# Kernel tuning notes

Measured on AMD Instinct MI355X. Metric: run time of the kernel, lower is better.

Reference implementation:

```python
import jax, jax.numpy as jnp
import numpy as np

D_MODEL = 2048
NUM_HEADS = 16
HEAD_DIM = D_MODEL // NUM_HEADS


def _rotary(x, head_dim):
    # x: (..., T, head_dim). Matches torch module: half-split rotation.
    T = x.shape[-2]
    pos = jnp.arange(T, dtype=jnp.float32)[:, None]              # (T,1)
    dim = jnp.arange(head_dim // 2, dtype=jnp.float32)[None, :]  # (1,hd/2)
    angle = pos * (1.0 / jnp.power(10000.0, 2.0 * dim / head_dim))
    cos = jnp.cos(angle)  # (T, hd/2), broadcasts over leading dims
    sin = jnp.sin(angle)
    x1 = x[..., : head_dim // 2]
    x2 = x[..., head_dim // 2:]
    return jnp.concatenate([x1 * cos - x2 * sin, x2 * cos + x1 * sin], axis=-1)


def setup_inputs() -> dict:
    key = jax.random.key(0)
    ks = jax.random.split(key, 9)
    B, T, D, H, HD = 2, 2048, D_MODEL, NUM_HEADS, HEAD_DIM
    s = 1.0 / np.sqrt(D)
    return {
        "x": jax.random.normal(ks[0], (B, T, D), jnp.float32),
        "Wq": jax.random.normal(ks[1], (D, D), jnp.float32) * s,
        "bq": jnp.zeros((D,), jnp.float32),
        "Wk": jax.random.normal(ks[2], (D, HD), jnp.float32) * s,
        "bk": jnp.zeros((HD,), jnp.float32),
        "Wv": jax.random.normal(ks[3], (D, HD), jnp.float32) * s,
        "bv": jnp.zeros((HD,), jnp.float32),
        "Wo": jax.random.normal(ks[4], (D, D), jnp.float32) * s,
        "bo": jnp.zeros((D,), jnp.float32),
    }


def reference(x, Wq, bq, Wk, bk, Wv, bv, Wo, bo):
    B, T, D = x.shape
    H, HD = NUM_HEADS, HEAD_DIM
    q = (x @ Wq + bq).reshape(B, T, H, HD).transpose(0, 2, 1, 3)  # (B,H,T,hd)
    k = (x @ Wk + bk)[:, None]                                    # (B,1,T,hd)
    v = (x @ Wv + bv)[:, None]                                    # (B,1,T,hd)
    q = _rotary(q, HD)
    k = _rotary(k, HD)
    scores = jnp.einsum("bhqd,bhkd->bhqk", q, jnp.broadcast_to(k, (B, 1, T, HD))) / jnp.sqrt(jnp.float32(HD))
    attn = jax.nn.softmax(scores, axis=-1)                        # (B,H,T,T)
    ctx = jnp.einsum("bhqk,bhkd->bhqd", attn, jnp.broadcast_to(v, (B, 1, T, HD)))
    ctx = ctx.transpose(0, 2, 1, 3).reshape(B, T, D)
    return ctx @ Wo + bo
```

## Files before the change

### kernel.cpp

```cpp
#include <hip/hip_runtime.h>
#include <math.h>

#define T_SEQ  2048
#define DMODEL 2048
#define NHEADS 16
#define HDIM   128
#define MROWS  4096

typedef __attribute__((ext_vector_type(8)))  __bf16 bf16x8;
typedef __attribute__((ext_vector_type(4)))  __bf16 bf16x4;
typedef __attribute__((ext_vector_type(4)))  float  f32x4;
typedef __attribute__((ext_vector_type(16))) float  f32x16;

#define GLOBAL_AS __attribute__((address_space(1)))
#define LDS_AS    __attribute__((address_space(3)))
__device__ __forceinline__ void async_copy16(const __bf16* g, __bf16* l) {
  __builtin_amdgcn_global_load_lds((const GLOBAL_AS void*)g, (LDS_AS void*)l, 16, 0, 0);
}

__global__ void build_rope_kernel(float2* __restrict__ rope) {
  int idx = blockIdx.x * blockDim.x + threadIdx.x;
  int d = idx & 63, pos = idx >> 6;
  double freq = pow(10000.0, -(double)d / 64.0);
  double ang = (double)pos * freq;
  rope[idx] = make_float2((float)cos(ang), (float)sin(ang));
}

__global__ void cast_bf16_kernel(const float* __restrict__ in,
                                 __bf16* __restrict__ out, int n4) {
  int i = blockIdx.x * blockDim.x + threadIdx.x;
  if (i >= n4) return;
  float4 v = ((const float4*)in)[i];
  bf16x4 o = { (__bf16)v.x, (__bf16)v.y, (__bf16)v.z, (__bf16)v.w };
  *(bf16x4*)(out + (size_t)i*4) = o;
}

__global__ void wtrans_kernel(const float* __restrict__ Wq,
                              const float* __restrict__ Wk,
                              const float* __restrict__ Wv,
                              const float* __restrict__ Wo,
                              __bf16* __restrict__ wqkvt,
                              __bf16* __restrict__ wot) {
  __shared__ float t[32][33];
  const int bx = blockIdx.x;
  const float* src; __bf16* dst; int istride, c0, orow;
  if (bx < 64)       { src = Wq; istride = 2048; c0 = bx*32;      orow = c0;        dst = wqkvt; }
  else if (bx < 68)  { src = Wk; istride = 128;  c0 = (bx-64)*32; orow = 2048 + c0; dst = wqkvt; }
  else if (bx < 72)  { src = Wv; istride = 128;  c0 = (bx-68)*32; orow = 2176 + c0; dst = wqkvt; }
  else               { src = Wo; istride = 2048; c0 = (bx-72)*32; orow = c0;        dst = wot; }
  const int tx = threadIdx.x & 31, ty = threadIdx.x >> 5;
  const int r0 = blockIdx.y*32;
#pragma unroll
  for (int i = 0; i < 4; ++i)
    t[ty + i*8][tx] = src[(size_t)(r0 + ty + i*8)*istride + c0 + tx];
  __syncthreads();
#pragma unroll
  for (int i = 0; i < 4; ++i)
    dst[(size_t)(orow + ty + i*8)*2048 + r0 + tx] = (__bf16)t[tx][ty + i*8];
}

__global__ void transpose_v_kernel(const __bf16* __restrict__ in,
                                   __bf16* __restrict__ out) {
  __shared__ __bf16 t[32][34];
  const int bz = blockIdx.z;
  in  += (size_t)bz * 2048 * 128;
  out += (size_t)bz * 128 * 2048;
  const int tx = threadIdx.x & 31, ty = threadIdx.x >> 5;
  const int r0 = blockIdx.y*32, c0 = blockIdx.x*32;
#pragma unroll
  for (int i = 0; i < 4; ++i)
    t[ty + i*8][tx] = in[(size_t)(r0 + ty + i*8)*128 + c0 + tx];
  __syncthreads();
#pragma unroll
  for (int i = 0; i < 4; ++i)
    out[(size_t)(c0 + ty + i*8)*2048 + r0 + tx] = t[tx][ty + i*8];
}

__global__ __launch_bounds__(256) void gemm_qkv_fused(
    const __bf16* __restrict__ A,
    const __bf16* __restrict__ Bt,
    const float* __restrict__ bq, const float* __restrict__ bk,
    const float* __restrict__ bv,
    const float2* __restrict__ rope,
    __bf16* __restrict__ qrb,
    __bf16* __restrict__ kbb,
    __bf16* __restrict__ vbb,
    float qscale)
{
  __shared__ __bf16 As[128*32];
  __shared__ __bf16 Bs[128*32];
  const int tid = threadIdx.x;
  const int lane = tid & 63, wave = tid >> 6;
  const int quad = lane >> 4, l16 = lane & 15;
  const int m0 = (wave >> 1)*64, n0 = (wave & 1)*32;
  const int row0 = blockIdx.y*128, col0 = blockIdx.x*128;
  const int srow = lane >> 2, scol = (lane & 3)*8;

  f32x4 acc[4][4];
#pragma unroll
  for (int i = 0; i < 4; ++i)
#pragma unroll
    for (int j = 0; j < 4; ++j) acc[i][j] = (f32x4){0.f,0.f,0.f,0.f};

  const __bf16* Ag = A  + (size_t)(row0 + wave*32 + srow)*DMODEL + scol;
  const __bf16* Bg = Bt + (size_t)(col0 + wave*32 + srow)*DMODEL + scol;
  __bf16* AsW = &As[wave*1024];
  __bf16* BsW = &Bs[wave*1024];

  for (int kk = 0; kk < DMODEL; kk += 32) {
    __syncthreads();
    async_copy16(Ag + kk,                     AsW);
    async_copy16(Ag + kk + (size_t)16*DMODEL, AsW + 512);
    async_copy16(Bg + kk,                     BsW);
    async_copy16(Bg + kk + (size_t)16*DMODEL, BsW + 512);
    __syncthreads();
    bf16x8 af[4], bfr[4];
#pragma unroll
    for (int i = 0; i < 4; ++i)
      af[i] = *(const bf16x8*)&As[(m0 + i*16 + l16)*32 + quad*8];
#pragma unroll
    for (int j = 0; j < 4; ++j) {
      const int cb = n0 + (j & 1)*16 + (j >> 1)*64;
      bfr[j] = *(const bf16x8*)&Bs[(cb + l16)*32 + quad*8];
    }
#pragma unroll
    for (int i = 0; i < 4; ++i)
#pragma unroll
      for (int j = 0; j < 4; ++j)
        acc[i][j] = __builtin_amdgcn_mfma_f32_16x16x32_bf16(af[i], bfr[j], acc[i][j], 0,0,0);
  }

  const int bx = blockIdx.x;
  const float* bias_p; float scale; bool rot; __bf16* obase; int ostride;
  if (bx < 16)      { bias_p = bq + bx*128; scale = qscale; rot = true;
                      obase = qrb + bx*128; ostride = 2048; }
  else if (bx == 16){ bias_p = bk; scale = 1.f; rot = true;
                      obase = kbb; ostride = 128; }
  else              { bias_p = bv; scale = 1.f; rot = false;
                      obase = vbb; ostride = 128; }

#pragma unroll
  for (int j = 0; j < 2; ++j) {
    const int d = n0 + j*16 + l16;
    const float b1 = bias_p[d], b2 = bias_p[d + 64];
#pragma unroll
    for (int i = 0; i < 4; ++i) {
      const int rl = m0 + i*16 + quad*4;
#pragma unroll
      for (int r = 0; r < 4; ++r) {
        const int rg = row0 + rl + r;
        const float x1 = acc[i][j][r]   + b1;
        const float x2 = acc[i][j+2][r] + b2;
        float c = 1.f, s = 0.f;
        if (rot) { float2 cs = rope[(size_t)(rg & (T_SEQ-1))*64 + d]; c = cs.x; s = cs.y; }
        obase[(size_t)rg*ostride + d]      = (__bf16)((x1*c - x2*s)*scale);
        obase[(size_t)rg*ostride + d + 64] = (__bf16)((x2*c + x1*s)*scale);
      }
    }
  }
}

__global__ __launch_bounds__(256) void gemm_bf16_t128(
    const __bf16* __restrict__ A, const __bf16* __restrict__ Bt,
    const float* __restrict__ bias, float* __restrict__ C,
    int M, int N, int K)
{
  __shared__ __bf16 As[128*32];
  __shared__ __bf16 Bs[128*32];
  const int tid = threadIdx.x;
  const int lane = tid & 63, wave = tid >> 6;
  const int quad = lane >> 4, l16 = lane & 15;
  const int m0 = (wave & 1)*64, n0 = (wave >> 1)*64;
  const int row0 = blockIdx.y*128, col0 = blockIdx.x*128;
  const int srow = lane >> 2, scol = (lane & 3)*8;

  f32x4 acc[4][4];
#pragma unroll
  for (int i = 0; i < 4; ++i)
#pragma unroll
    for (int j = 0; j < 4; ++j) acc[i][j] = (f32x4){0.f,0.f,0.f,0.f};

  const __bf16* Ag = A  + (size_t)(row0 + wave*32 + srow)*K + scol;
  const __bf16* Bg = Bt + (size_t)(col0 + wave*32 + srow)*K + scol;
  __bf16* AsW = &As[wave*1024];
  __bf16* BsW = &Bs[wave*1024];

  for (int kk = 0; kk < K; kk += 32) {
    __syncthreads();
    async_copy16(Ag + kk,              AsW);
    async_copy16(Ag + kk + (size_t)16*K, AsW + 512);
    async_copy16(Bg + kk,              BsW);
    async_copy16(Bg + kk + (size_t)16*K, BsW + 512);
    __syncthreads();
    bf16x8 af[4], bfr[4];
#pragma unroll
    for (int i = 0; i < 4; ++i)
      af[i] = *(const bf16x8*)&As[(m0 + i*16 + l16)*32 + quad*8];
#pragma unroll
    for (int j = 0; j < 4; ++j)
      bfr[j] = *(const bf16x8*)&Bs[(n0 + j*16 + l16)*32 + quad*8];
#pragma unroll
    for (int i = 0; i < 4; ++i)
#pragma unroll
      for (int j = 0; j < 4; ++j)
        acc[i][j] = __builtin_amdgcn_mfma_f32_16x16x32_bf16(af[i], bfr[j], acc[i][j], 0,0,0);
  }
#pragma unroll
  for (int j = 0; j < 4; ++j) {
    const int ccol = col0 + n0 + j*16 + l16;
    const float bvv = bias[ccol];
#pragma unroll
    for (int i = 0; i < 4; ++i) {
      const int crow = row0 + m0 + i*16 + quad*4;
#pragma unroll
      for (int r = 0; r < 4; ++r)
        C[(size_t)(crow + r)*N + ccol] = acc[i][j][r] + bvv;
    }
  }
}

#define KSTR 136
#define VSTR 72
#define PSTR 72
__global__ __launch_bounds__(256) void mqa_attn_mfma(
    const __bf16* __restrict__ qb,
    const __bf16* __restrict__ kb,
    const __bf16* __restrict__ vt,
    __bf16* __restrict__ ctx)
{
  __shared__ __bf16 Ks[64*KSTR];
  __shared__ __bf16 Vs[128*VSTR];
  __shared__ __bf16 Ps[4][32*PSTR];
  __shared__ float  Linv[128];
  const int tid = threadIdx.x, lane = tid & 63, wave = tid >> 6;
  const int h5 = lane >> 5, l32 = lane & 31;
  const int h = blockIdx.y, b = blockIdx.z;
  const int qbase = blockIdx.x*128 + wave*32;

  bf16x8 qf[8];
  const __bf16* qp = qb + ((size_t)b*T_SEQ + qbase + l32)*DMODEL + h*HDIM;
#pragma unroll
  for (int ds = 0; ds < 8; ++ds) qf[ds] = *(const bf16x8*)(qp + ds*16 + h5*8);

  f32x16 oacc[4];
#pragma unroll
  for (int g = 0; g < 4; ++g)
#pragma unroll
    for (int r = 0; r < 16; ++r) oacc[g][r] = 0.f;
  float lsum = 0.f;

  const __bf16* kbase = kb + (size_t)b*T_SEQ*HDIM;
  const __bf16* vbase = vt + (size_t)b*HDIM*T_SEQ;

  for (int kt = 0; kt < T_SEQ/64; ++kt) {
    __syncthreads();
#pragma unroll
    for (int i = 0; i < 4; ++i) {
      int idx = i*256 + tid;
      int key = idx >> 4, c = idx & 15;
      *(bf16x8*)&Ks[key*KSTR + c*8] =
          *(const bf16x8*)(kbase + (size_t)(kt*64 + key)*HDIM + c*8);
    }
#pragma unroll
    for (int i = 0; i < 4; ++i) {
      int idx = i*256 + tid;
      int d = idx >> 3, c = idx & 7;
      *(bf16x8*)&Vs[d*VSTR + c*8] =
          *(const bf16x8*)(vbase + (size_t)d*T_SEQ + kt*64 + c*8);
    }
    __syncthreads();

    f32x16 sacc[2];
#pragma unroll
    for (int kg = 0; kg < 2; ++kg) {
#pragma unroll
      for (int r = 0; r < 16; ++r) sacc[kg][r] = 0.f;
#pragma unroll
      for (int ds = 0; ds < 8; ++ds) {
        bf16x8 kf = *(const bf16x8*)&Ks[(kg*32 + l32)*KSTR + ds*16 + h5*8];
        sacc[kg] = __builtin_amdgcn_mfma_f32_32x32x16_bf16(kf, qf[ds], sacc[kg], 0,0,0);
      }
    }
#pragma unroll
    for (int kg = 0; kg < 2; ++kg)
#pragma unroll
      for (int r1 = 0; r1 < 4; ++r1) {
        bf16x4 pk;
#pragma unroll
        for (int r0 = 0; r0 < 4; ++r0) {
          float p = __builtin_amdgcn_exp2f(sacc[kg][r1*4 + r0]);
          lsum += p;
          pk[r0] = (__bf16)p;
        }
        *(bf16x4*)&Ps[wave][l32*PSTR + kg*32 + r1*8 + h5*4] = pk;
      }
    __asm__ volatile("s_waitcnt lgkmcnt(0)" ::: "memory");
#pragma unroll
    for (int ks = 0; ks < 4; ++ks) {
      bf16x8 pf = *(const bf16x8*)&Ps[wave][l32*PSTR + ks*16 + h5*8];
#pragma unroll
      for (int g = 0; g < 4; ++g) {
        bf16x8 vf = *(const bf16x8*)&Vs[(g*32 + l32)*VSTR + ks*16 + h5*8];
        oacc[g] = __builtin_amdgcn_mfma_f32_32x32x16_bf16(pf, vf, oacc[g], 0,0,0);
      }
    }
  }

  lsum += __shfl_xor(lsum, 32);
  if (h5 == 0) Linv[wave*32 + l32] = 1.f / lsum;
  __asm__ volatile("s_waitcnt lgkmcnt(0)" ::: "memory");

  __bf16* op = ctx + ((size_t)b*T_SEQ + qbase)*DMODEL + h*HDIM + l32;
#pragma unroll
  for (int r1 = 0; r1 < 4; ++r1) {
    float4 iv = *(const float4*)&Linv[wave*32 + r1*8 + h5*4];
#pragma unroll
    for (int r0 = 0; r0 < 4; ++r0) {
      int qrow = r1*8 + h5*4 + r0;
#pragma unroll
      for (int g = 0; g < 4; ++g)
        op[(size_t)qrow*DMODEL + g*32] = (__bf16)(oacc[g][r1*4 + r0] * (&iv.x)[r0]);
    }
  }
}

extern "C" void kernel_launch(void* const* d_in, const int* in_sizes, int n_in,
                              void* d_out, int out_size, void* d_ws, size_t ws_size,
                              hipStream_t stream) {
  const float* x  = (const float*)d_in[0];
  const float* Wq = (const float*)d_in[1];
  const float* bq = (const float*)d_in[2];
  const float* Wk = (const float*)d_in[3];
  const float* bk = (const float*)d_in[4];
  const float* Wv = (const float*)d_in[5];
  const float* bv = (const float*)d_in[6];
  const float* Wo = (const float*)d_in[7];
  const float* bo = (const float*)d_in[8];
  float* out = (float*)d_out;

  uint8_t* ws = (uint8_t*)d_ws;
  __bf16* qrb  = (__bf16*)(ws);
  __bf16* xb   = (__bf16*)(ws + 16777216);
  __bf16* wqkvt= (__bf16*)(ws + 33554432);
  __bf16* wot  = (__bf16*)(ws + 42991616);
  __bf16* kbb  = (__bf16*)(ws + 51380224);
  __bf16* vbb  = (__bf16*)(ws + 52428800);
  __bf16* vtb  = (__bf16*)(ws + 53477376);
  float2* rope = (float2*)(ws + 54525952);

  const float qscale = 1.4426950408889634f * 0.08838834764831845f;

  build_rope_kernel<<<512, 256, 0, stream>>>(rope);
  wtrans_kernel<<<dim3(136,64), 256, 0, stream>>>(Wq, Wk, Wv, Wo, wqkvt, wot);
  cast_bf16_kernel<<<8192, 256, 0, stream>>>(x, xb, MROWS*DMODEL/4);

  gemm_qkv_fused<<<dim3(18,32), 256, 0, stream>>>(
      xb, wqkvt, bq, bk, bv, rope, qrb, kbb, vbb, qscale);

  transpose_v_kernel<<<dim3(4,64,2), 256, 0, stream>>>(vbb, vtb);

  mqa_attn_mfma<<<dim3(16,16,2), 256, 0, stream>>>(qrb, kbb, vtb, xb);

  gemm_bf16_t128<<<dim3(16,32), 256, 0, stream>>>(xb, wot, bo, out, MROWS, DMODEL, DMODEL);
}
```

Before: 314.0 us.

## Keep attention probabilities in registers via permuted K rows, drop LDS P staging

The K-tile row index is permuted so the S=K·Q^T MFMA output layout lines up with the B-operand layout needed for the P·V MFMA. The exp'd scores then go straight from registers into the PV product, and the transposed product O^T=V^T·P^T is accumulated. This removes the per-tile LDS write/read of P and its waitcnt barrier. The epilogue becomes per-query-row vectorized bf16x4 stores without the Linv LDS exchange. Correctness depends on the bit permutation exactly matching the MFMA register layouts.

```diff
diff --git a/kernel.cpp b/kernel.cpp
--- a/kernel.cpp
+++ b/kernel.cpp
@@ -221,7 +221,6 @@
 
 #define KSTR 136
 #define VSTR 72
-#define PSTR 72
 __global__ __launch_bounds__(256) void mqa_attn_mfma(
     const __bf16* __restrict__ qb,
     const __bf16* __restrict__ kb,
@@ -230,10 +229,9 @@
 {
   __shared__ __bf16 Ks[64*KSTR];
   __shared__ __bf16 Vs[128*VSTR];
-  __shared__ __bf16 Ps[4][32*PSTR];
-  __shared__ float  Linv[128];
   const int tid = threadIdx.x, lane = tid & 63, wave = tid >> 6;
   const int h5 = lane >> 5, l32 = lane & 31;
+  const int swr = (l32 & 19) | ((l32 & 4) << 1) | ((l32 & 8) >> 1);
   const int h = blockIdx.y, b = blockIdx.z;
   const int qbase = blockIdx.x*128 + wave*32;
 
@@ -270,58 +268,46 @@
     }
     __syncthreads();
 
-    f32x16 sacc[2];
 #pragma unroll
     for (int kg = 0; kg < 2; ++kg) {
-#pragma unroll
-      for (int r = 0; r < 16; ++r) sacc[kg][r] = 0.f;
+      f32x16 sacc;
+#pragma unroll
+      for (int r = 0; r < 16; ++r) sacc[r] = 0.f;
 #pragma unroll
       for (int ds = 0; ds < 8; ++ds) {
-        bf16x8 kf = *(const bf16x8*)&Ks[(kg*32 + l32)*KSTR + ds*16 + h5*8];
-        sacc[kg] = __builtin_amdgcn_mfma_f32_32x32x16_bf16(kf, qf[ds], sacc[kg], 0,0,0);
+        bf16x8 kf = *(const bf16x8*)&Ks[(kg*32 + swr)*KSTR + ds*16 + h5*8];
+        sacc = __builtin_amdgcn_mfma_f32_32x32x16_bf16(kf, qf[ds], sacc, 0,0,0);
       }
-    }
-#pragma unroll
-    for (int kg = 0; kg < 2; ++kg)
-#pragma unroll
-      for (int r1 = 0; r1 < 4; ++r1) {
-        bf16x4 pk;
-#pragma unroll
-        for (int r0 = 0; r0 < 4; ++r0) {
-          float p = __builtin_amdgcn_exp2f(sacc[kg][r1*4 + r0]);
-          lsum += p;
-          pk[r0] = (__bf16)p;
+      bf16x8 pf[2];
+#pragma unroll
+      for (int r = 0; r < 16; ++r) {
+        float p = __builtin_amdgcn_exp2f(sacc[r]);
+        lsum += p;
+        pf[r >> 3][r & 7] = (__bf16)p;
+      }
+#pragma unroll
+      for (int ks = 0; ks < 2; ++ks)
+#pragma unroll
+        for (int g = 0; g < 4; ++g) {
+          bf16x8 vf = *(const bf16x8*)&Vs[(g*32 + l32)*VSTR + kg*32 + ks*16 + h5*8];
+          oacc[g] = __builtin_amdgcn_mfma_f32_32x32x16_bf16(vf, pf[ks], oacc[g], 0,0,0);
         }
-        *(bf16x4*)&Ps[wave][l32*PSTR + kg*32 + r1*8 + h5*4] = pk;
-      }
-    __asm__ volatile("s_waitcnt lgkmcnt(0)" ::: "memory");
-#pragma unroll
-    for (int ks = 0; ks < 4; ++ks) {
-      bf16x8 pf = *(const bf16x8*)&Ps[wave][l32*PSTR + ks*16 + h5*8];
-#pragma unroll
-      for (int g = 0; g < 4; ++g) {
-        bf16x8 vf = *(const bf16x8*)&Vs[(g*32 + l32)*VSTR + ks*16 + h5*8];
-        oacc[g] = __builtin_amdgcn_mfma_f32_32x32x16_bf16(pf, vf, oacc[g], 0,0,0);
-      }
     }
   }
 
   lsum += __shfl_xor(lsum, 32);
-  if (h5 == 0) Linv[wave*32 + l32] = 1.f / lsum;
-  __asm__ volatile("s_waitcnt lgkmcnt(0)" ::: "memory");
-
-  __bf16* op = ctx + ((size_t)b*T_SEQ + qbase)*DMODEL + h*HDIM + l32;
-#pragma unroll
-  for (int r1 = 0; r1 < 4; ++r1) {
-    float4 iv = *(const float4*)&Linv[wave*32 + r1*8 + h5*4];
-#pragma unroll
-    for (int r0 = 0; r0 < 4; ++r0) {
-      int qrow = r1*8 + h5*4 + r0;
-#pragma unroll
-      for (int g = 0; g < 4; ++g)
-        op[(size_t)qrow*DMODEL + g*32] = (__bf16)(oacc[g][r1*4 + r0] * (&iv.x)[r0]);
-    }
-  }
+  const float inv = 1.f / lsum;
+
+  __bf16* op = ctx + ((size_t)b*T_SEQ + qbase + l32)*DMODEL + h*HDIM;
+#pragma unroll
+  for (int g = 0; g < 4; ++g)
+#pragma unroll
+    for (int rq = 0; rq < 4; ++rq) {
+      const int d = g*32 + rq*8 + h5*4;
+      bf16x4 ov = { (__bf16)(oacc[g][rq*4+0]*inv), (__bf16)(oacc[g][rq*4+1]*inv),
+                    (__bf16)(oacc[g][rq*4+2]*inv), (__bf16)(oacc[g][rq*4+3]*inv) };
+      *(bf16x4*)&op[d] = ov;
+    }
 }
 
 extern "C" void kernel_launch(void* const* d_in, const int* in_sizes, int n_in,
```

Measured after the change: 360.7 us. 1.15x slower.
